# Kernel tuning notes

Hardware: AMD Instinct MI355X
Metric: run time of the kernel (lower is better)

The kernel has to match this reference:

```python
import jax, jax.numpy as jnp
import numpy as np

H1, W1 = 16, 16  # SparseAttBlock stride
EPS = 1e-5       # BatchNorm eps


def _att(x, wx, bx, wy, by, wo, bo, gamma, beta):
    """DotProductAttBlock: 1x1 q/k projections, full softmax attention over
    the H*W tokens of each (small) block, then 1x1 conv + BatchNorm(train) + ReLU."""
    B, C, H, W = x.shape
    xf = x.reshape(B, C, H * W)                                  # [B,C,N]
    theta = jnp.einsum('mc,bcn->bnm', wx, xf) + bx               # [B,N,fmid]
    psi = jnp.einsum('mc,bcn->bmn', wy, xf) + by[:, None]        # [B,fmid,N]
    alpha = jax.nn.softmax(jnp.einsum('bnm,bmk->bnk', theta, psi), axis=2)  # [B,N,N]
    agg = jnp.einsum('bnk,bck->bcn', alpha, xf)                  # [B,C,N]
    out = jnp.einsum('oc,bcn->bon', wo, agg) + bo[:, None]       # [B,fout,N]
    # BatchNorm2d in training mode: biased batch stats over (batch, spatial)
    mean = out.mean(axis=(0, 2), keepdims=True)
    var = ((out - mean) ** 2).mean(axis=(0, 2), keepdims=True)
    out = (out - mean) * jax.lax.rsqrt(var + EPS) * gamma[:, None] + beta[:, None]
    return jax.nn.relu(out).reshape(B, -1, H, W)


def _forward(x, p1, p2):
    B, C, H, W = x.shape
    h2, w2 = H // H1, W // W1
    # pass 1: attention within each (H1,W1) block, blocks folded into batch
    xb = x.reshape(B, C, H1, h2, W1, w2).transpose(0, 3, 5, 1, 2, 4)
    xb = xb.reshape(B * h2 * w2, C, H1, W1)
    xb = _att(xb, *p1)
    # pass 2: attention across the (h2,w2) block grid
    xb = xb.reshape(B, h2, w2, C, H1, W1).transpose(0, 4, 5, 3, 1, 2)
    xb = xb.reshape(B * H1 * W1, C, h2, w2)
    xb = _att(xb, *p2)
    return xb.reshape(B, H1, W1, C, h2, w2).transpose(0, 3, 1, 4, 2, 5).reshape(B, C, H, W)


def setup_inputs() -> dict:
    key = jax.random.key(0)
    ks = jax.random.split(key, 20)
    B, C, FMID, H, W = 4, 128, 64, 256, 256
    s = 0.05
    d = {'x': jax.random.normal(ks[0], (B, C, H, W), jnp.float32)}
    d['w1x'] = jax.random.normal(ks[1], (FMID, C), jnp.float32) * s
    d['b1x'] = jax.random.normal(ks[2], (FMID,), jnp.float32) * s
    d['w1y'] = jax.random.normal(ks[3], (FMID, C), jnp.float32) * s
    d['b1y'] = jax.random.normal(ks[4], (FMID,), jnp.float32) * s
    d['w1o'] = jax.random.normal(ks[5], (C, C), jnp.float32) * s
    d['b1o'] = jax.random.normal(ks[6], (C,), jnp.float32) * s
    d['g1'] = jnp.ones((C,), jnp.float32)
    d['be1'] = jnp.zeros((C,), jnp.float32)
    d['w2x'] = jax.random.normal(ks[7], (FMID, C), jnp.float32) * s
    d['b2x'] = jax.random.normal(ks[8], (FMID,), jnp.float32) * s
    d['w2y'] = jax.random.normal(ks[9], (FMID, C), jnp.float32) * s
    d['b2y'] = jax.random.normal(ks[10], (FMID,), jnp.float32) * s
    d['w2o'] = jax.random.normal(ks[11], (C, C), jnp.float32) * s
    d['b2o'] = jax.random.normal(ks[12], (C,), jnp.float32) * s
    d['g2'] = jnp.ones((C,), jnp.float32)
    d['be2'] = jnp.zeros((C,), jnp.float32)
    return d


def reference(x, w1x, b1x, w1y, b1y, w1o, b1o, g1, be1,
              w2x, b2x, w2y, b2y, w2o, b2o, g2, be2):
    p1 = (w1x, b1x, w1y, b1y, w1o, b1o, g1, be1)
    p2 = (w2x, b2x, w2y, b2y, w2o, b2o, g2, be2)
    return _forward(x, p1, p2)
```

## Files before the change

### kernel.cpp

```cpp
#include <hip/hip_runtime.h>

typedef _Float16 f16;
typedef f16 f16x2 __attribute__((ext_vector_type(2)));
typedef f16 f16x4 __attribute__((ext_vector_type(4)));
typedef f16 f16x8 __attribute__((ext_vector_type(8)));
typedef float f32x4 __attribute__((ext_vector_type(4)));
typedef float f32x16 __attribute__((ext_vector_type(16)));
typedef unsigned int u32;
typedef u32 u32x2 __attribute__((ext_vector_type(2)));
typedef u32 u32x4 __attribute__((ext_vector_type(4)));

#define MFMA32(a, b, c) __builtin_amdgcn_mfma_f32_32x32x16_f16((a), (b), (c), 0, 0, 0)

__device__ __forceinline__ u32 pk2(float a, float b) {
    return __builtin_bit_cast(u32, __builtin_amdgcn_cvt_pkrtz(a, b));
}
__device__ __forceinline__ f16x4 pk4(float a, float b, float c, float d) {
    u32x2 t = {pk2(a, b), pk2(c, d)};
    return __builtin_bit_cast(f16x4, t);
}
__device__ __forceinline__ f16x4 lo4(f16x8 v) { return __builtin_shufflevector(v, v, 0, 1, 2, 3); }
__device__ __forceinline__ f16x4 hi4(f16x8 v) { return __builtin_shufflevector(v, v, 4, 5, 6, 7); }

#define OFF_Y   65536
#define OFF_SC  98304
#define OFF_SST 131072
#define LDS_ATT 132096

__global__ __launch_bounds__(512) void repack_kernel(const float* __restrict__ x,
                                                     f16* __restrict__ Xall) {
    __shared__ f16 XT[128 * 264];
    const int tid = threadIdx.x, g = blockIdx.x;
    const int b = g >> 8, i1 = (g >> 4) & 15, i2 = g & 15;
    const int h = i1 * 16 + i2;
    {
        const int c = tid >> 2, wq = (tid & 3) * 64;
        const float* src = x + (((size_t)b * 128 + c) * 256 + h) * 256 + wq;
        f16* dst = XT + c * 264 + wq;
#pragma unroll
        for (int i = 0; i < 16; ++i) {
            f32x4 v = *(const f32x4*)(src + i * 4);
            f16x4 o = {(f16)v[0], (f16)v[1], (f16)v[2], (f16)v[3]};
            *(f16x4*)(dst + i * 4) = o;
        }
    }
    __syncthreads();
    {
        const int w = tid >> 1, ch = (tid & 1) * 64;
        const int j1 = w >> 4, j2 = w & 15;
        f16* dst = Xall + (((size_t)b * 256 + i2 * 16 + j2) * 256 + i1 * 16 + j1) * 128 + ch;
#pragma unroll
        for (int i = 0; i < 8; ++i) {
            f16x8 v;
#pragma unroll
            for (int j = 0; j < 8; ++j) v[j] = XT[(ch + i * 8 + j) * 264 + w];
            *(f16x8*)(dst + i * 8) = v;
        }
    }
}

__global__ void wconv_kernel(const float* __restrict__ w1x, const float* __restrict__ w1y,
                             const float* __restrict__ w1o, const float* __restrict__ w2x,
                             const float* __restrict__ w2y, const float* __restrict__ w2o,
                             f16* __restrict__ Wf) {
    int i = blockIdx.x * 256 + threadIdx.x;
    int p = i >> 15, idx = i & 32767;
    int j = idx & 7, lane = (idx >> 3) & 63, ks = (idx >> 9) & 7, r = idx >> 12;
    int row = r * 32 + (lane & 31);
    int c = ks * 16 + (lane >> 5) * 8 + j;
    const float* s;
    if (p == 0) s = (row < 128) ? w1o + row * 128 : (row < 192) ? w1x + (row - 128) * 128
                                                               : w1y + (row - 192) * 128;
    else        s = (row < 128) ? w2o + row * 128 : (row < 192) ? w2x + (row - 128) * 128
                                                               : w2y + (row - 192) * 128;
    Wf[i] = (f16)s[c];
}

template <int PASS>
__global__ __launch_bounds__(512, 2) void att_kernel(
    const f16* __restrict__ Xin, const f16* __restrict__ Wf, const float* __restrict__ bq,
    const float* __restrict__ bk, const float* __restrict__ bo, const float* __restrict__ bnab,
    f16* __restrict__ Uout, float* __restrict__ gstats, int t_stride, int s_stride) {
    __shared__ __align__(16) char smem[LDS_ATT];
    float* SST = (float*)(smem + OFF_SST);
    const int tid = threadIdx.x;
    const int w = tid >> 6, l = tid & 63, hl = l >> 5, l31 = l & 31;
    const int g = blockIdx.x, R0 = w * 32;
    char* scb = smem + OFF_SC + w * 4096;

    if (tid < 256) SST[tid] = 0.f;

#pragma unroll
    for (int j = 0; j < 8; ++j) {
        int byte = (j * 512 + tid) * 16;
        *(f16x8*)(smem + byte) = *(const f16x8*)((const char*)Wf + byte);
    }

    const f16* src = Xin + (size_t)g * 32768 + (R0 + l31) * 128 + hl * 8;
    f16x8 afr[8];
#pragma unroll
    for (int ks = 0; ks < 8; ++ks) afr[ks] = *(const f16x8*)(src + ks * 16);
    if constexpr (PASS == 2) {
#pragma unroll
        for (int ks = 0; ks < 8; ++ks) {
            const int c0 = ks * 16 + hl * 8;
            f32x4 a0 = *(const f32x4*)(bnab + c0), a1 = *(const f32x4*)(bnab + c0 + 4);
            f32x4 s0 = *(const f32x4*)(bnab + 128 + c0), s1 = *(const f32x4*)(bnab + 132 + c0);
            f16x8 v = afr[ks];
#pragma unroll
            for (int j = 0; j < 4; ++j) {
                v[j]     = (f16)fmaxf(a0[j] * (float)v[j]     + s0[j], 0.f);
                v[j + 4] = (f16)fmaxf(a1[j] * (float)v[j + 4] + s1[j], 0.f);
            }
            afr[ks] = v;
        }
    }
    __syncthreads();

    f32x16 aT[2] = {}, aP[2] = {};
#pragma unroll
    for (int ks = 0; ks < 8; ++ks)
#pragma unroll
        for (int nt = 0; nt < 2; ++nt) {
            f16x8 Bq = *(const f16x8*)(smem + (((4 + nt) * 8 + ks) * 64 + l) * 16);
            f16x8 Bk = *(const f16x8*)(smem + (((6 + nt) * 8 + ks) * 64 + l) * 16);
            aT[nt] = MFMA32(afr[ks], Bq, aT[nt]);
            aP[nt] = MFMA32(afr[ks], Bk, aP[nt]);
        }
    {
        const int lf = (l31 >> 3) & 1;
        const int msub = l31 >> 4;
        const int jb = (l31 & 7) * 2;
#pragma unroll
        for (int nt = 0; nt < 2; ++nt) {
            float bqv = bq[nt * 32 + l31], bkv = bk[nt * 32 + l31];
            char* bT = scb + (((nt * 2 + msub) * 64) + 32 * lf) * 16 + jb;
            char* bY = smem + OFF_Y + (((w * 4 + nt * 2 + msub) * 64) + 32 * lf) * 16 + jb;
#pragma unroll
            for (int r = 0; r < 16; ++r) {
                int tl = (r & 3) + 8 * (r >> 2) + 4 * hl;
                *(f16*)(bT + tl * 16) = (f16)(aT[nt][r] + bqv);
                *(f16*)(bY + tl * 16) = (f16)(aP[nt][r] + bkv);
            }
        }
    }
    f16x8 tb[4];
#pragma unroll
    for (int ks = 0; ks < 4; ++ks) tb[ks] = *(const f16x8*)(scb + (ks * 64 + l) * 16);

    f32x16 aV[4] = {};
#pragma unroll
    for (int ks = 0; ks < 8; ++ks)
#pragma unroll
        for (int ct = 0; ct < 4; ++ct) {
            f16x8 Bo = *(const f16x8*)(smem + ((ct * 8 + ks) * 64 + l) * 16);
            aV[ct] = MFMA32(afr[ks], Bo, aV[ct]);
        }
    __syncthreads();

#pragma unroll
    for (int ct = 0; ct < 4; ++ct) {
        float bov = bo[ct * 32 + l31];
#pragma unroll
        for (int q = 0; q < 4; ++q) {
            int ts = 2 * w + (q >> 1);
            f16x4 pv = pk4(aV[ct][4 * q + 0] + bov, aV[ct][4 * q + 1] + bov,
                           aV[ct][4 * q + 2] + bov, aV[ct][4 * q + 3] + bov);
            *(f16x4*)(smem + (((ts * 4 + ct) * 64) + l31 + 32 * (q & 1)) * 16 + 8 * hl) = pv;
        }
    }
    __syncthreads();

    f32x16 s[8] = {};
    __builtin_amdgcn_s_setprio(1);
#pragma unroll
    for (int kt = 0; kt < 8; ++kt)
#pragma unroll
        for (int ks = 0; ks < 4; ++ks) {
            f16x8 ay = *(const f16x8*)(smem + OFF_Y + (((kt * 4 + ks) * 64) + l) * 16);
            s[kt] = MFMA32(ay, tb[ks], s[kt]);
        }
    __builtin_amdgcn_s_setprio(0);

    float mx = -1e30f;
#pragma unroll
    for (int kt = 0; kt < 8; ++kt) {
        float m0 = fmaxf(fmaxf(s[kt][0], s[kt][1]), fmaxf(s[kt][2], s[kt][3]));
        float m1 = fmaxf(fmaxf(s[kt][4], s[kt][5]), fmaxf(s[kt][6], s[kt][7]));
        float m2 = fmaxf(fmaxf(s[kt][8], s[kt][9]), fmaxf(s[kt][10], s[kt][11]));
        float m3 = fmaxf(fmaxf(s[kt][12], s[kt][13]), fmaxf(s[kt][14], s[kt][15]));
        mx = fmaxf(mx, fmaxf(fmaxf(m0, m1), fmaxf(m2, m3)));
    }
    mx = fmaxf(mx, __shfl_xor(mx, 32));
    float sum = 0.f;
#pragma unroll
    for (int kt = 0; kt < 8; ++kt)
#pragma unroll
        for (int e = 0; e < 16; ++e) {
            float p = __expf(s[kt][e] - mx);
            s[kt][e] = p;
            sum += p;
        }
    sum += __shfl_xor(sum, 32);
    const float rs = 1.f / sum;

    f32x16 o[4] = {};
#pragma unroll
    for (int kt = 0; kt < 8; ++kt) {
#pragma unroll
        for (int ks = 0; ks < 2; ++ks) {
            u32 a0 = pk2(s[kt][8 * ks + 0] * rs, s[kt][8 * ks + 1] * rs);
            u32 a1 = pk2(s[kt][8 * ks + 2] * rs, s[kt][8 * ks + 3] * rs);
            u32 b0 = pk2(s[kt][8 * ks + 4] * rs, s[kt][8 * ks + 5] * rs);
            u32 b1 = pk2(s[kt][8 * ks + 6] * rs, s[kt][8 * ks + 7] * rs);
            u32x2 r0 = __builtin_amdgcn_permlane32_swap(a0, b0, false, false);
            u32x2 r1 = __builtin_amdgcn_permlane32_swap(a1, b1, false, false);
            u32x4 aw = {r0.x, r1.x, r0.y, r1.y};
            f16x8 ap = __builtin_bit_cast(f16x8, aw);
            __builtin_amdgcn_s_setprio(1);
#pragma unroll
            for (int ct = 0; ct < 4; ++ct) {
                f16x8 bv = *(const f16x8*)(smem + ((((kt * 2 + ks) * 4 + ct) * 64) + l) * 16);
                o[ct] = MFMA32(ap, bv, o[ct]);
            }
            __builtin_amdgcn_s_setprio(0);
        }
    }

#pragma unroll
    for (int ct = 0; ct < 4; ++ct) {
        float ss = 0.f, sq = 0.f;
#pragma unroll
        for (int e = 0; e < 16; ++e) {
            float v = o[ct][e];
            ss += v;
            sq += v * v;
        }
        ss += __shfl_xor(ss, 32);
        sq += __shfl_xor(sq, 32);
        if (hl == 0) {
            atomicAdd(&SST[ct * 32 + l31], ss);
            atomicAdd(&SST[128 + ct * 32 + l31], sq);
        }
    }

    const size_t ub = (size_t)(g >> 8) * 8388608 + (size_t)(g & 255) * (size_t)s_stride;
#pragma unroll
    for (int ro = 0; ro < 2; ++ro) {
#pragma unroll
        for (int ct = 0; ct < 4; ++ct)
#pragma unroll
            for (int rr = 0; rr < 8; ++rr) {
                int r = ro * 8 + rr;
                int tl2 = (r & 3) + 8 * ((r >> 2) & 1) + 4 * hl;
                int c = ct * 32 + l31;
                *(f16*)(scb + ((tl2 * 256 + c * 2) ^ (((tl2 >> 2) & 3) << 4))) = (f16)o[ct][r];
            }
#pragma unroll
        for (int i = 0; i < 4; ++i) {
            int row = i * 4 + (l >> 4);
            f16x8 v8 = *(const f16x8*)(scb + ((row * 256 + (l & 15) * 16) ^
                                              (((row >> 2) & 3) << 4)));
            int t = R0 + ro * 16 + row;
            *(f16x8*)(Uout + ub + (size_t)t * (size_t)t_stride + (l & 15) * 8) = v8;
        }
    }
    __syncthreads();
    if (tid < 256) atomicAdd(&gstats[tid], SST[tid]);
}

__global__ void bnfix_kernel(const float* __restrict__ gstats, const float* __restrict__ gamma,
                             const float* __restrict__ beta, float* __restrict__ ab) {
    int c = threadIdx.x;
    if (c < 128) {
        const float inv = 1.f / 262144.f;
        float mean = gstats[c] * inv;
        float var = gstats[128 + c] * inv - mean * mean;
        float rstd = rsqrtf(var + 1e-5f);
        float a = gamma[c] * rstd;
        ab[c] = a;
        ab[128 + c] = beta[c] - mean * a;
    }
}

__global__ __launch_bounds__(256) void final_kernel(const f16* __restrict__ U2,
                                                    const float* __restrict__ ab,
                                                    float* __restrict__ out) {
    __shared__ f16 L[256 * 132];
    const int tid = threadIdx.x, g = blockIdx.x;
    const int b = g >> 8, i1 = (g >> 4) & 15, j1 = g & 15;
    const f16* src = U2 + (size_t)g * 32768;
#pragma unroll
    for (int e = 0; e < 16; ++e) {
        int u = e * 2048 + tid * 8;
        int row = u >> 7, c0 = u & 127;
        f16x8 v = *(const f16x8*)(src + u);
        f16* dst = L + row * 132 + c0;
        *(f16x4*)dst = lo4(v);
        *(f16x4*)(dst + 4) = hi4(v);
    }
    __syncthreads();
    const int j2 = tid & 15, bu = tid >> 4;
#pragma unroll 4
    for (int k = 0; k < 128; ++k) {
        int unit = bu + k * 16;
        int c = unit & 127, i2 = unit >> 7;
        float a = ab[c], bb = ab[128 + c];
        float v = fmaxf(a * (float)L[(i2 * 16 + j2) * 132 + c] + bb, 0.f);
        out[(((size_t)b * 128 + c) * 256 + i1 * 16 + i2) * 256 + j1 * 16 + j2] = v;
    }
}

extern "C" void kernel_launch(void* const* d_in, const int* in_sizes, int n_in, void* d_out,
                              int out_size, void* d_ws, size_t ws_size, hipStream_t stream) {
    (void)in_sizes; (void)n_in; (void)out_size; (void)ws_size;
    const float* x = (const float*)d_in[0];
    const float* w1x = (const float*)d_in[1];
    const float* b1x = (const float*)d_in[2];
    const float* w1y = (const float*)d_in[3];
    const float* b1y = (const float*)d_in[4];
    const float* w1o = (const float*)d_in[5];
    const float* b1o = (const float*)d_in[6];
    const float* g1 = (const float*)d_in[7];
    const float* be1 = (const float*)d_in[8];
    const float* w2x = (const float*)d_in[9];
    const float* b2x = (const float*)d_in[10];
    const float* w2y = (const float*)d_in[11];
    const float* b2y = (const float*)d_in[12];
    const float* w2o = (const float*)d_in[13];
    const float* b2o = (const float*)d_in[14];
    const float* g2 = (const float*)d_in[15];
    const float* be2 = (const float*)d_in[16];

    f16* Xall = (f16*)d_out;
    f16* U1 = (f16*)((char*)d_out + 67108864);
    f16* U2 = (f16*)d_ws;
    f16* Wbf = (f16*)((char*)d_ws + 67108864);
    float* gstats = (float*)((char*)d_ws + 67108864 + 262144);
    float* bnab = gstats + 512;

    (void)hipMemsetAsync(gstats, 0, 2048, stream);
    wconv_kernel<<<256, 256, 0, stream>>>(w1x, w1y, w1o, w2x, w2y, w2o, Wbf);
    repack_kernel<<<1024, 512, 0, stream>>>(x, Xall);

    att_kernel<1><<<1024, 512, 0, stream>>>(Xall, Wbf, b1x, b1y, b1o, (const float*)nullptr, U1,
                                            gstats, 32768, 128);
    bnfix_kernel<<<1, 128, 0, stream>>>(gstats, g1, be1, bnab);
    att_kernel<2><<<1024, 512, 0, stream>>>(U1, Wbf + 32768, b2x, b2y, b2o, bnab, U2,
                                            gstats + 256, 128, 32768);
    bnfix_kernel<<<1, 128, 0, stream>>>(gstats + 256, g2, be2, bnab + 256);
    final_kernel<<<1024, 256, 0, stream>>>(U2, bnab + 256, (float*)d_out);
}
```

Before: 269.4 us.

## Transpose projection MFMAs to build operand fragments in registers via permlane swaps

Swaps the operand order of the q/k projection MFMAs so the accumulator layout can be turned directly into f16x8 MFMA operand fragments with permlane32_swap. This removes the per-wave scratch LDS region and the scalar f16 LDS stores and reloads. Biases are pre-converted to f16 and appended to the weight buffer. The output write-back now stores scalar f16 straight to global memory instead of staging through swizzled LDS. LDS use per block drops, but the global stores become narrow 2-byte writes, which may coalesce worse.

```diff
diff --git a/kernel.cpp b/kernel.cpp
--- a/kernel.cpp
+++ b/kernel.cpp
@@ -15,17 +15,31 @@
 __device__ __forceinline__ u32 pk2(float a, float b) {
     return __builtin_bit_cast(u32, __builtin_amdgcn_cvt_pkrtz(a, b));
 }
-__device__ __forceinline__ f16x4 pk4(float a, float b, float c, float d) {
-    u32x2 t = {pk2(a, b), pk2(c, d)};
-    return __builtin_bit_cast(f16x4, t);
-}
 __device__ __forceinline__ f16x4 lo4(f16x8 v) { return __builtin_shufflevector(v, v, 0, 1, 2, 3); }
 __device__ __forceinline__ f16x4 hi4(f16x8 v) { return __builtin_shufflevector(v, v, 4, 5, 6, 7); }
 
+__device__ __forceinline__ f16x8 xfrm(f32x16 v, int rb) {
+    u32 a0 = pk2(v[rb + 0], v[rb + 1]);
+    u32 a1 = pk2(v[rb + 2], v[rb + 3]);
+    u32 b0 = pk2(v[rb + 4], v[rb + 5]);
+    u32 b1 = pk2(v[rb + 6], v[rb + 7]);
+    u32x2 r0 = __builtin_amdgcn_permlane32_swap(a0, b0, false, false);
+    u32x2 r1 = __builtin_amdgcn_permlane32_swap(a1, b1, false, false);
+    u32x4 aw = {r0.x, r1.x, r0.y, r1.y};
+    return __builtin_bit_cast(f16x8, aw);
+}
+__device__ __forceinline__ f16x8 add8(f16x8 a, f16x8 b) {
+    f16x8 r;
+#pragma unroll
+    for (int j = 0; j < 8; ++j) r[j] = a[j] + b[j];
+    return r;
+}
+
 #define OFF_Y   65536
-#define OFF_SC  98304
-#define OFF_SST 131072
-#define LDS_ATT 132096
+#define OFF_SST 98304
+#define LDS_ATT 99328
+
+#define WSTRIDE 32896
 
 __global__ __launch_bounds__(512) void repack_kernel(const float* __restrict__ x,
                                                      f16* __restrict__ Xall) {
@@ -60,33 +74,41 @@
 }
 
 __global__ void wconv_kernel(const float* __restrict__ w1x, const float* __restrict__ w1y,
-                             const float* __restrict__ w1o, const float* __restrict__ w2x,
+                             const float* __restrict__ w1o, const float* __restrict__ b1x,
+                             const float* __restrict__ b1y, const float* __restrict__ w2x,
                              const float* __restrict__ w2y, const float* __restrict__ w2o,
+                             const float* __restrict__ b2x, const float* __restrict__ b2y,
                              f16* __restrict__ Wf) {
     int i = blockIdx.x * 256 + threadIdx.x;
-    int p = i >> 15, idx = i & 32767;
-    int j = idx & 7, lane = (idx >> 3) & 63, ks = (idx >> 9) & 7, r = idx >> 12;
-    int row = r * 32 + (lane & 31);
-    int c = ks * 16 + (lane >> 5) * 8 + j;
-    const float* s;
-    if (p == 0) s = (row < 128) ? w1o + row * 128 : (row < 192) ? w1x + (row - 128) * 128
-                                                               : w1y + (row - 192) * 128;
-    else        s = (row < 128) ? w2o + row * 128 : (row < 192) ? w2x + (row - 128) * 128
-                                                               : w2y + (row - 192) * 128;
-    Wf[i] = (f16)s[c];
+    if (i < 65536) {
+        int p = i >> 15, idx = i & 32767;
+        int j = idx & 7, lane = (idx >> 3) & 63, ks = (idx >> 9) & 7, r = idx >> 12;
+        int row = r * 32 + (lane & 31);
+        int c = ks * 16 + (lane >> 5) * 8 + j;
+        const float* s;
+        if (p == 0) s = (row < 128) ? w1o + row * 128 : (row < 192) ? w1x + (row - 128) * 128
+                                                                   : w1y + (row - 192) * 128;
+        else        s = (row < 128) ? w2o + row * 128 : (row < 192) ? w2x + (row - 128) * 128
+                                                                   : w2y + (row - 192) * 128;
+        Wf[p * WSTRIDE + idx] = (f16)s[c];
+    } else {
+        int idx2 = i - 65536;
+        int p = idx2 >> 7, r = idx2 & 127;
+        const float* bsrc = (p == 0) ? ((r < 64) ? b1x : b1y) : ((r < 64) ? b2x : b2y);
+        Wf[p * WSTRIDE + 32768 + r] = (f16)bsrc[r & 63];
+    }
 }
 
 template <int PASS>
 __global__ __launch_bounds__(512, 2) void att_kernel(
-    const f16* __restrict__ Xin, const f16* __restrict__ Wf, const float* __restrict__ bq,
-    const float* __restrict__ bk, const float* __restrict__ bo, const float* __restrict__ bnab,
-    f16* __restrict__ Uout, float* __restrict__ gstats, int t_stride, int s_stride) {
+    const f16* __restrict__ Xin, const f16* __restrict__ Wf, const float* __restrict__ bo,
+    const float* __restrict__ bnab, f16* __restrict__ Uout, float* __restrict__ gstats,
+    int t_stride, int s_stride) {
     __shared__ __align__(16) char smem[LDS_ATT];
     float* SST = (float*)(smem + OFF_SST);
     const int tid = threadIdx.x;
     const int w = tid >> 6, l = tid & 63, hl = l >> 5, l31 = l & 31;
     const int g = blockIdx.x, R0 = w * 32;
-    char* scb = smem + OFF_SC + w * 4096;
 
     if (tid < 256) SST[tid] = 0.f;
 
@@ -115,60 +137,68 @@
             afr[ks] = v;
         }
     }
-    __syncthreads();
-
-    f32x16 aT[2] = {}, aP[2] = {};
+
+    const f16* bf = Wf + 32768;
+    f16x8 bqf[4], bkf[4];
+#pragma unroll
+    for (int ks = 0; ks < 4; ++ks) {
+        bqf[ks] = *(const f16x8*)(bf + ks * 16 + hl * 8);
+        bkf[ks] = *(const f16x8*)(bf + 64 + ks * 16 + hl * 8);
+    }
+    __syncthreads();
+
+    {
+        f32x16 aP[2] = {};
+#pragma unroll
+        for (int ks = 0; ks < 8; ++ks)
+#pragma unroll
+            for (int mt = 0; mt < 2; ++mt) {
+                f16x8 wk = *(const f16x8*)(smem + (((6 + mt) * 8 + ks) * 64 + l) * 16);
+                aP[mt] = MFMA32(wk, afr[ks], aP[mt]);
+            }
+#pragma unroll
+        for (int ks = 0; ks < 4; ++ks) {
+            f16x8 yf = add8(xfrm(aP[ks >> 1], 8 * (ks & 1)), bkf[ks]);
+            *(f16x8*)(smem + OFF_Y + ((w * 4 + ks) * 64 + l) * 16) = yf;
+        }
+    }
+
+    f16x8 tb[4];
+    {
+        f32x16 aT[2] = {};
+#pragma unroll
+        for (int ks = 0; ks < 8; ++ks)
+#pragma unroll
+            for (int mt = 0; mt < 2; ++mt) {
+                f16x8 wq = *(const f16x8*)(smem + (((4 + mt) * 8 + ks) * 64 + l) * 16);
+                aT[mt] = MFMA32(wq, afr[ks], aT[mt]);
+            }
+#pragma unroll
+        for (int ks = 0; ks < 4; ++ks)
+            tb[ks] = add8(xfrm(aT[ks >> 1], 8 * (ks & 1)), bqf[ks]);
+    }
+
+    f32x16 aV[4] = {};
 #pragma unroll
     for (int ks = 0; ks < 8; ++ks)
 #pragma unroll
-        for (int nt = 0; nt < 2; ++nt) {
-            f16x8 Bq = *(const f16x8*)(smem + (((4 + nt) * 8 + ks) * 64 + l) * 16);
-            f16x8 Bk = *(const f16x8*)(smem + (((6 + nt) * 8 + ks) * 64 + l) * 16);
-            aT[nt] = MFMA32(afr[ks], Bq, aT[nt]);
-            aP[nt] = MFMA32(afr[ks], Bk, aP[nt]);
-        }
-    {
-        const int lf = (l31 >> 3) & 1;
-        const int msub = l31 >> 4;
-        const int jb = (l31 & 7) * 2;
-#pragma unroll
-        for (int nt = 0; nt < 2; ++nt) {
-            float bqv = bq[nt * 32 + l31], bkv = bk[nt * 32 + l31];
-            char* bT = scb + (((nt * 2 + msub) * 64) + 32 * lf) * 16 + jb;
-            char* bY = smem + OFF_Y + (((w * 4 + nt * 2 + msub) * 64) + 32 * lf) * 16 + jb;
-#pragma unroll
-            for (int r = 0; r < 16; ++r) {
-                int tl = (r & 3) + 8 * (r >> 2) + 4 * hl;
-                *(f16*)(bT + tl * 16) = (f16)(aT[nt][r] + bqv);
-                *(f16*)(bY + tl * 16) = (f16)(aP[nt][r] + bkv);
-            }
-        }
-    }
-    f16x8 tb[4];
-#pragma unroll
-    for (int ks = 0; ks < 4; ++ks) tb[ks] = *(const f16x8*)(scb + (ks * 64 + l) * 16);
-
-    f32x16 aV[4] = {};
-#pragma unroll
-    for (int ks = 0; ks < 8; ++ks)
-#pragma unroll
         for (int ct = 0; ct < 4; ++ct) {
-            f16x8 Bo = *(const f16x8*)(smem + ((ct * 8 + ks) * 64 + l) * 16);
-            aV[ct] = MFMA32(afr[ks], Bo, aV[ct]);
-        }
-    __syncthreads();
-
+            f16x8 wo = *(const f16x8*)(smem + ((ct * 8 + ks) * 64 + l) * 16);
+            aV[ct] = MFMA32(afr[ks], wo, aV[ct]);
+        }
 #pragma unroll
     for (int ct = 0; ct < 4; ++ct) {
         float bov = bo[ct * 32 + l31];
 #pragma unroll
-        for (int q = 0; q < 4; ++q) {
-            int ts = 2 * w + (q >> 1);
-            f16x4 pv = pk4(aV[ct][4 * q + 0] + bov, aV[ct][4 * q + 1] + bov,
-                           aV[ct][4 * q + 2] + bov, aV[ct][4 * q + 3] + bov);
-            *(f16x4*)(smem + (((ts * 4 + ct) * 64) + l31 + 32 * (q & 1)) * 16 + 8 * hl) = pv;
-        }
-    }
+        for (int e = 0; e < 16; ++e) aV[ct][e] += bov;
+    }
+    __syncthreads();
+
+#pragma unroll
+    for (int ct = 0; ct < 4; ++ct)
+#pragma unroll
+        for (int ksl = 0; ksl < 2; ++ksl)
+            *(f16x8*)(smem + (((2 * w + ksl) * 4 + ct) * 64 + l) * 16) = xfrm(aV[ct], 8 * ksl);
     __syncthreads();
 
     f32x16 s[8] = {};
@@ -177,7 +207,7 @@
     for (int kt = 0; kt < 8; ++kt)
 #pragma unroll
         for (int ks = 0; ks < 4; ++ks) {
-            f16x8 ay = *(const f16x8*)(smem + OFF_Y + (((kt * 4 + ks) * 64) + l) * 16);
+            f16x8 ay = *(const f16x8*)(smem + OFF_Y + ((kt * 4 + ks) * 64 + l) * 16);
             s[kt] = MFMA32(ay, tb[ks], s[kt]);
         }
     __builtin_amdgcn_s_setprio(0);
@@ -203,29 +233,25 @@
         }
     sum += __shfl_xor(sum, 32);
     const float rs = 1.f / sum;
+#pragma unroll
+    for (int kt = 0; kt < 8; ++kt)
+#pragma unroll
+        for (int e = 0; e < 16; ++e) s[kt][e] *= rs;
 
     f32x16 o[4] = {};
 #pragma unroll
-    for (int kt = 0; kt < 8; ++kt) {
-#pragma unroll
-        for (int ks = 0; ks < 2; ++ks) {
-            u32 a0 = pk2(s[kt][8 * ks + 0] * rs, s[kt][8 * ks + 1] * rs);
-            u32 a1 = pk2(s[kt][8 * ks + 2] * rs, s[kt][8 * ks + 3] * rs);
-            u32 b0 = pk2(s[kt][8 * ks + 4] * rs, s[kt][8 * ks + 5] * rs);
-            u32 b1 = pk2(s[kt][8 * ks + 6] * rs, s[kt][8 * ks + 7] * rs);
-            u32x2 r0 = __builtin_amdgcn_permlane32_swap(a0, b0, false, false);
-            u32x2 r1 = __builtin_amdgcn_permlane32_swap(a1, b1, false, false);
-            u32x4 aw = {r0.x, r1.x, r0.y, r1.y};
-            f16x8 ap = __builtin_bit_cast(f16x8, aw);
+    for (int kt = 0; kt < 8; ++kt)
+#pragma unroll
+        for (int ks2 = 0; ks2 < 2; ++ks2) {
+            f16x8 ap = xfrm(s[kt], 8 * ks2);
             __builtin_amdgcn_s_setprio(1);
 #pragma unroll
             for (int ct = 0; ct < 4; ++ct) {
-                f16x8 bv = *(const f16x8*)(smem + ((((kt * 2 + ks) * 4 + ct) * 64) + l) * 16);
+                f16x8 bv = *(const f16x8*)(smem + (((kt * 2 + ks2) * 4 + ct) * 64 + l) * 16);
                 o[ct] = MFMA32(ap, bv, o[ct]);
             }
             __builtin_amdgcn_s_setprio(0);
         }
-    }
 
 #pragma unroll
     for (int ct = 0; ct < 4; ++ct) {
@@ -246,24 +272,11 @@
 
     const size_t ub = (size_t)(g >> 8) * 8388608 + (size_t)(g & 255) * (size_t)s_stride;
 #pragma unroll
-    for (int ro = 0; ro < 2; ++ro) {
-#pragma unroll
-        for (int ct = 0; ct < 4; ++ct)
-#pragma unroll
-            for (int rr = 0; rr < 8; ++rr) {
-                int r = ro * 8 + rr;
-                int tl2 = (r & 3) + 8 * ((r >> 2) & 1) + 4 * hl;
-                int c = ct * 32 + l31;
-                *(f16*)(scb + ((tl2 * 256 + c * 2) ^ (((tl2 >> 2) & 3) << 4))) = (f16)o[ct][r];
-            }
-#pragma unroll
-        for (int i = 0; i < 4; ++i) {
-            int row = i * 4 + (l >> 4);
-            f16x8 v8 = *(const f16x8*)(scb + ((row * 256 + (l & 15) * 16) ^
-                                              (((row >> 2) & 3) << 4)));
-            int t = R0 + ro * 16 + row;
-            *(f16x8*)(Uout + ub + (size_t)t * (size_t)t_stride + (l & 15) * 8) = v8;
-        }
+    for (int r = 0; r < 16; ++r) {
+        int trow = (r & 3) + 8 * (r >> 2) + 4 * hl;
+        f16* rp = Uout + ub + (size_t)(R0 + trow) * (size_t)t_stride + l31;
+#pragma unroll
+        for (int ct = 0; ct < 4; ++ct) rp[ct * 32] = (f16)o[ct][r];
     }
     __syncthreads();
     if (tid < 256) atomicAdd(&gstats[tid], SST[tid]);
@@ -340,14 +353,14 @@
     float* bnab = gstats + 512;
 
     (void)hipMemsetAsync(gstats, 0, 2048, stream);
-    wconv_kernel<<<256, 256, 0, stream>>>(w1x, w1y, w1o, w2x, w2y, w2o, Wbf);
+    wconv_kernel<<<257, 256, 0, stream>>>(w1x, w1y, w1o, b1x, b1y, w2x, w2y, w2o, b2x, b2y, Wbf);
     repack_kernel<<<1024, 512, 0, stream>>>(x, Xall);
 
-    att_kernel<1><<<1024, 512, 0, stream>>>(Xall, Wbf, b1x, b1y, b1o, (const float*)nullptr, U1,
-                                            gstats, 32768, 128);
+    att_kernel<1><<<1024, 512, 0, stream>>>(Xall, Wbf, b1o, (const float*)nullptr, U1, gstats,
+                                            32768, 128);
     bnfix_kernel<<<1, 128, 0, stream>>>(gstats, g1, be1, bnab);
-    att_kernel<2><<<1024, 512, 0, stream>>>(U1, Wbf + 32768, b2x, b2y, b2o, bnab, U2,
-                                            gstats + 256, 128, 32768);
+    att_kernel<2><<<1024, 512, 0, stream>>>(U1, Wbf + WSTRIDE, b2o, bnab, U2, gstats + 256, 128,
+                                            32768);
     bnfix_kernel<<<1, 128, 0, stream>>>(gstats + 256, g2, be2, bnab + 256);
     final_kernel<<<1024, 256, 0, stream>>>(U2, bnab + 256, (float*)d_out);
 }
```

New measurement: 271.8 us. No clear change (+0.9%).
